# Optimization experiments

Measured on AMD Instinct MI355X. Metric: run time of the kernel, lower is better.

The kernel has to match this reference:

```python
import jax, jax.numpy as jnp
import numpy as np

N_EMBD = 256
BLOCK_SIZE = 128
N_HEAD = 8
HEAD_SIZE = 256
B = 256
T = 128


def setup_inputs() -> dict:
    key = jax.random.key(0)
    ks = jax.random.split(key, 9)
    s = 0.02
    return {
        "x": jax.random.normal(ks[0], (B, T, N_EMBD), dtype=jnp.float32),
        # torch Linear weight layout: [out_features, in_features], stacked over heads
        "Wq": jax.random.normal(ks[1], (N_HEAD, HEAD_SIZE, N_EMBD), dtype=jnp.float32) * s,
        "bq": jax.random.normal(ks[2], (N_HEAD, HEAD_SIZE), dtype=jnp.float32) * s,
        "Wk": jax.random.normal(ks[3], (N_HEAD, HEAD_SIZE, N_EMBD), dtype=jnp.float32) * s,
        "bk": jax.random.normal(ks[4], (N_HEAD, HEAD_SIZE), dtype=jnp.float32) * s,
        "Wv": jax.random.normal(ks[5], (N_HEAD, HEAD_SIZE, N_EMBD), dtype=jnp.float32) * s,
        "bv": jax.random.normal(ks[6], (N_HEAD, HEAD_SIZE), dtype=jnp.float32) * s,
        "Wp": jax.random.normal(ks[7], (N_EMBD, N_EMBD), dtype=jnp.float32) * s,
        "bp": jax.random.normal(ks[8], (N_EMBD,), dtype=jnp.float32) * s,
    }


def reference(x, Wq, bq, Wk, bk, Wv, bv, Wp, bp):
    Bb, Tt, C = x.shape
    scale = C ** (-0.5)  # NOTE: original scales by n_embd (input C), not head_size
    # per-head projections: [h, b, t, d]
    q = jnp.einsum("btc,hdc->hbtd", x, Wq) + bq[:, None, None, :]
    k = jnp.einsum("btc,hdc->hbtd", x, Wk) + bk[:, None, None, :]
    v = jnp.einsum("btc,hdc->hbtd", x, Wv) + bv[:, None, None, :]
    att = jnp.einsum("hbtd,hbsd->hbts", q, k) * scale  # [h,b,t,s]
    causal = jnp.tril(jnp.ones((Tt, Tt), dtype=bool))
    att = jnp.where(causal, att, -jnp.inf)
    att = jax.nn.softmax(att, axis=-1)
    out = jnp.einsum("hbts,hbsd->hbtd", att, v)
    # torch.cat along dim=0 (batch concat, as written in the source)
    out = out.reshape(out.shape[0] * Bb, Tt, out.shape[-1])  # [h*b, t, head_size]
    return out @ Wp.T + bp
```

## Files before the change

### kernel.cpp

```cpp
#include <hip/hip_runtime.h>
#include <hip/hip_bf16.h>
#include <stdint.h>


#define TT 128

typedef __attribute__((ext_vector_type(8))) short short8;
typedef __attribute__((ext_vector_type(4))) float f32x4;

#define WS_X    0u
#define WS_M    16777216u
#define WS_WM   17825792u
#define WS_WB   18874368u
#define WS_BB   18939904u
#define WS_CQ   18948096u

#define LX     0
#define LT     65536
#define LP     65536
#define LH     98304
#define R_UV   131072
#define R_RED  132096
#define LDS_SIZE 134144

#define VMCNT0() asm volatile("s_waitcnt vmcnt(0)" ::: "memory")
#define LGKM0()  asm volatile("s_waitcnt lgkmcnt(0)" ::: "memory")
#define BAR()    do { asm volatile("" ::: "memory"); __builtin_amdgcn_s_barrier(); asm volatile("" ::: "memory"); } while (0)
#define PRIO1()  __builtin_amdgcn_s_setprio(1)
#define PRIO0()  __builtin_amdgcn_s_setprio(0)

typedef __attribute__((address_space(3))) uint32_t lds_u32;
typedef __attribute__((address_space(1))) const uint32_t glb_u32;

__device__ __forceinline__ unsigned short f2bf(float x) {
    union { float f; unsigned u; } v; v.f = x;
    unsigned r = v.u + 0x7FFFu + ((v.u >> 16) & 1u);
    return (unsigned short)(r >> 16);
}
__device__ __forceinline__ unsigned pk2(float a, float b) {
    return (unsigned)f2bf(a) | ((unsigned)f2bf(b) << 16);
}

__global__ __launch_bounds__(256) void convert_pre(
    const float* __restrict__ x,
    const float* __restrict__ Wq, const float* __restrict__ bq,
    const float* __restrict__ Wk, const float* __restrict__ bk,
    const float* __restrict__ Wv, const float* __restrict__ bv,
    const float* __restrict__ Wp, const float* __restrict__ bp,
    char* __restrict__ ws)
{
    extern __shared__ char clds[];
    const int tid = threadIdx.x;
    const int bid = blockIdx.x;

    if (bid < 256) {
        const float* src = x + (size_t)bid * 32768;
        char* dst = ws + WS_X + (size_t)bid * 65536;
        for (int i = tid; i < 8192; i += 256) {
            float4 v = ((const float4*)src)[i];
            int row = i >> 6, c4 = i & 63;
            uint2 u; u.x = pk2(v.x, v.y); u.y = pk2(v.z, v.w);
            *(uint2*)(clds + row * 512 + ((c4 * 8) ^ ((row & 7) << 4))) = u;
        }
        __syncthreads();
        for (int i = tid; i < 4096; i += 256) {
            int l = i & 63, ks = (i >> 6) & 7, g = i >> 9;
            int r = g * 16 + (l & 15);
            int boff = ks * 64 + (l >> 4) * 16;
            uint4 q = *(const uint4*)(clds + r * 512 + (boff ^ ((r & 7) << 4)));
            ((uint4*)dst)[i] = q;
        }
        return;
    }
    if (bid < 384) {
        int id = bid - 256, h = id >> 4, st = id & 15;
        float* wkL = (float*)clds;
        for (int i = tid; i < 4096; i += 256) {
            int d = i >> 4, cc = i & 15;
            wkL[i] = Wk[(size_t)h * 65536 + d * 256 + st * 16 + cc];
        }
        __syncthreads();
        const int c = tid;
        float4 a0 = {0,0,0,0}, a1 = {0,0,0,0}, a2 = {0,0,0,0}, a3 = {0,0,0,0};
        const float4* wk4 = (const float4*)wkL;
        #pragma unroll 4
        for (int d = 0; d < 256; ++d) {
            float a = Wq[(size_t)h * 65536 + d * 256 + c];
            float4 k0 = wk4[d*4+0], k1 = wk4[d*4+1], k2 = wk4[d*4+2], k3 = wk4[d*4+3];
            a0.x += a*k0.x; a0.y += a*k0.y; a0.z += a*k0.z; a0.w += a*k0.w;
            a1.x += a*k1.x; a1.y += a*k1.y; a1.z += a*k1.z; a1.w += a*k1.w;
            a2.x += a*k2.x; a2.y += a*k2.y; a2.z += a*k2.z; a2.w += a*k2.w;
            a3.x += a*k3.x; a3.y += a*k3.y; a3.z += a*k3.z; a3.w += a*k3.w;
        }
        float acc[16] = {a0.x,a0.y,a0.z,a0.w, a1.x,a1.y,a1.z,a1.w,
                         a2.x,a2.y,a2.z,a2.w, a3.x,a3.y,a3.z,a3.w};
        char* base = ws + WS_M + (size_t)h * 131072;
        int ks = c >> 5, lgp = (c >> 3) & 3, jb = c & 7;
        #pragma unroll
        for (int j = 0; j < 16; ++j) {
            int cp = st * 16 + j;
            *(unsigned short*)(base + (((st * 8 + ks)) << 10)
                + ((cp & 15) + 16 * lgp) * 16 + jb * 2) = f2bf(acc[j] * 0.0625f);
        }
        return;
    }
    if (bid < 512) {
        int id = bid - 384, h = id >> 4, st = id & 15;
        float* wpT2 = (float*)clds;
        for (int i = tid; i < 1024; i += 256) {
            int e = i >> 6, d4 = i & 63;
            float4 v = ((const float4*)(Wp + (size_t)(st * 16 + e) * 256))[d4];
            int d = d4 * 4;
            wpT2[(d+0)*20+e] = v.x; wpT2[(d+1)*20+e] = v.y;
            wpT2[(d+2)*20+e] = v.z; wpT2[(d+3)*20+e] = v.w;
        }
        __syncthreads();
        const int c = tid;
        float4 a0 = {0,0,0,0}, a1 = {0,0,0,0}, a2 = {0,0,0,0}, a3 = {0,0,0,0};
        #pragma unroll 4
        for (int d = 0; d < 256; ++d) {
            float wv = Wv[(size_t)h * 65536 + d * 256 + c];
            const float4* wp4 = (const float4*)(wpT2 + d * 20);
            float4 p0 = wp4[0], p1 = wp4[1], p2 = wp4[2], p3 = wp4[3];
            a0.x += wv*p0.x; a0.y += wv*p0.y; a0.z += wv*p0.z; a0.w += wv*p0.w;
            a1.x += wv*p1.x; a1.y += wv*p1.y; a1.z += wv*p1.z; a1.w += wv*p1.w;
            a2.x += wv*p2.x; a2.y += wv*p2.y; a2.z += wv*p2.z; a2.w += wv*p2.w;
            a3.x += wv*p3.x; a3.y += wv*p3.y; a3.z += wv*p3.z; a3.w += wv*p3.w;
        }
        float acc[16] = {a0.x,a0.y,a0.z,a0.w, a1.x,a1.y,a1.z,a1.w,
                         a2.x,a2.y,a2.z,a2.w, a3.x,a3.y,a3.z,a3.w};
        char* base = ws + WS_WM + (size_t)h * 131072;
        int ks = c >> 5, lgp = (c >> 3) & 3, jb = c & 7;
        #pragma unroll
        for (int j = 0; j < 16; ++j) {
            *(unsigned short*)(base + (((st * 8 + ks)) << 10)
                + (j + 16 * lgp) * 16 + jb * 2) = f2bf(acc[j]);
        }
        return;
    }
    if (bid < 520) {
        const int h = bid - 512;
        {
            uint4 z = {0u,0u,0u,0u};
            for (int i = tid; i < 512; i += 256)
                ((uint4*)(ws + WS_WB + (size_t)h * 8192))[i] = z;
        }
        float* tK = (float*)clds;
        float* tQ = (float*)(clds + 16384);
        const int c = tid;
        float s1 = 0.f, s2 = 0.f;
        for (int d0 = 0; d0 < 256; d0 += 16) {
            __syncthreads();
            for (int i = tid; i < 1024; i += 256) {
                int row = i >> 6, c4 = i & 63;
                ((float4*)tK)[row * 64 + c4] =
                    ((const float4*)(Wk + (size_t)h * 65536 + (size_t)(d0 + row) * 256))[c4];
                ((float4*)tQ)[row * 64 + c4] =
                    ((const float4*)(Wq + (size_t)h * 65536 + (size_t)(d0 + row) * 256))[c4];
            }
            __syncthreads();
            #pragma unroll
            for (int dd = 0; dd < 16; ++dd) {
                s1 += tK[dd * 256 + c] * bq[h * 256 + d0 + dd];
                s2 += tQ[dd * 256 + c] * bk[h * 256 + d0 + dd];
            }
        }
        int ks = c >> 5, lgp = (c >> 3) & 3, jb = c & 7;
        char* base = ws + WS_WB + (size_t)h * 8192 + ks * 1024;
        *(unsigned short*)(base + (0 + 16 * lgp) * 16 + jb * 2) = f2bf(s2 * 0.0625f);
        *(unsigned short*)(base + (1 + 16 * lgp) * 16 + jb * 2) = f2bf(s1 * 0.0625f);
        float* red = (float*)(clds + 32768);
        red[tid] = bq[h * 256 + tid] * bk[h * 256 + tid];
        __syncthreads();
        if (tid == 0) {
            float cq = 0.f;
            for (int d = 0; d < 256; ++d) cq += red[d];
            *(float*)(ws + WS_CQ + h * 4) = cq * 0.0625f;
        }
        return;
    }
    {
        const int st = bid - 520;
        float* wpT = (float*)clds;
        float* bvL = (float*)(clds + 17408);
        for (int i = tid; i < 1024; i += 256) {
            int row = i >> 6, c4 = i & 63;
            float4 v = ((const float4*)(Wp + (size_t)(st * 16 + row) * 256))[c4];
            float* dstp = wpT + row * 257 + c4 * 4;
            dstp[0] = v.x; dstp[1] = v.y; dstp[2] = v.z; dstp[3] = v.w;
        }
        for (int i = tid; i < 512; i += 256)
            ((float4*)bvL)[i] = ((const float4*)bv)[i];
        __syncthreads();
        const int el = tid >> 4, dg = tid & 15;
        #pragma unroll
        for (int h = 0; h < 8; ++h) {
            float p = 0.f;
            #pragma unroll
            for (int dd = 0; dd < 16; ++dd) {
                int d = dg * 16 + dd;
                p += bvL[h * 256 + d] * wpT[el * 257 + d];
            }
            p += __shfl_xor(p, 1);
            p += __shfl_xor(p, 2);
            p += __shfl_xor(p, 4);
            p += __shfl_xor(p, 8);
            if (dg == 0)
                *(float*)(ws + WS_BB + (size_t)h * 1024 + (st * 16 + el) * 4)
                    = bp[st * 16 + el] + p;
        }
        return;
    }
}

__global__ __launch_bounds__(1024, 1) void mha_fused(
    const char* __restrict__ ws, float* __restrict__ out)
{
    extern __shared__ char lds[];
    const int tid = threadIdx.x;
    const int w  = tid >> 6, l = tid & 63;
    const int lg = l >> 4, lr = l & 15;
    const int mq = w & 7, nh = w >> 3;
    const int bid = blockIdx.x;
    const int xcd = bid & 7, j = bid >> 3;
    const int h = j & 7;
    const int b = ((j >> 3) << 3) | xcd;
    const size_t orow = ((size_t)(h * 256 + b)) * TT;

    const char* Xf  = ws + WS_X  + (size_t)b * 65536;
    const char* Mh  = ws + WS_M  + (size_t)h * 131072;
    const char* WMh = ws + WS_WM + (size_t)h * 131072;
    const char* WBh = ws + WS_WB + (size_t)h * 8192;

    {
        const char* src = Xf + tid * 16;
        #pragma unroll
        for (int p = 0; p < 4; ++p)
            __builtin_amdgcn_global_load_lds((glb_u32*)(src + p * 16384),
                (lds_u32*)(lds + LX + tid * 16 + p * 16384), 16, 0, 0);
    }
    VMCNT0(); BAR();

    if (nh == 0) {
        f32x4 vacc = f32x4{0.f,0.f,0.f,0.f};
        #pragma unroll
        for (int ks = 0; ks < 8; ++ks) {
            short8 wb = *(const short8*)(WBh + (ks << 10) + l*16);
            short8 xa = *(const short8*)(lds + LX + (((mq*8 + ks)) << 10) + l*16);
            vacc = __builtin_amdgcn_mfma_f32_16x16x32_bf16(xa, wb, vacc, 0, 0, 0);
        }
        if (lr < 2) {
            #pragma unroll
            for (int r = 0; r < 4; ++r) {
                int t = mq*16 + lg*4 + r;
                *(float*)(lds + R_UV + lr*512 + t*4) = vacc[r];
            }
        }
    }

    {
        const int th = w >> 3, cp = w & 7;
        f32x4 acc[4][2];
        #pragma unroll
        for (int i = 0; i < 4; ++i)
            #pragma unroll
            for (int c2 = 0; c2 < 2; ++c2) acc[i][c2] = f32x4{0.f,0.f,0.f,0.f};
        #pragma unroll
        for (int ks = 0; ks < 8; ++ks) {
            short8 nb[2];
            #pragma unroll
            for (int c2 = 0; c2 < 2; ++c2)
                nb[c2] = *(const short8*)(Mh + ((((cp*2+c2)*8 + ks)) << 10) + l*16);
            short8 xa[4];
            #pragma unroll
            for (int i = 0; i < 4; ++i)
                xa[i] = *(const short8*)(lds + LX + ((((th*4+i)*8 + ks)) << 10) + l*16);
            PRIO1();
            #pragma unroll
            for (int i = 0; i < 4; ++i)
                #pragma unroll
                for (int c2 = 0; c2 < 2; ++c2)
                    acc[i][c2] = __builtin_amdgcn_mfma_f32_16x16x32_bf16(xa[i], nb[c2], acc[i][c2], 0, 0, 0);
            PRIO0();
        }
        #pragma unroll
        for (int i = 0; i < 4; ++i)
            #pragma unroll
            for (int c2 = 0; c2 < 2; ++c2)
                #pragma unroll
                for (int r = 0; r < 4; ++r) {
                    int t = (th*4+i)*16 + lg*4 + r;
                    int c = (cp*2+c2)*16 + lr;
                    *(unsigned short*)(lds + LT + t*512 + ((c*2) ^ ((t&7)<<4)))
                        = f2bf(acc[i][c2][r]);
                }
    }
    LGKM0(); BAR();

    f32x4 sacc[4];
    #pragma unroll
    for (int i = 0; i < 4; ++i) sacc[i] = f32x4{0.f,0.f,0.f,0.f};
    #pragma unroll
    for (int ks2 = 0; ks2 < 8; ++ks2) {
        int t2 = mq*16 + lr;
        short8 ta = *(const short8*)(lds + LT + t2*512 + ((ks2*64 + lg*16) ^ ((t2&7)<<4)));
        short8 sb[4];
        #pragma unroll
        for (int nt = 0; nt < 4; ++nt)
            sb[nt] = *(const short8*)(lds + LX + (((nh*4+nt)*8 + ks2) << 10) + l*16);
        PRIO1();
        #pragma unroll
        for (int nt = 0; nt < 4; ++nt)
            sacc[nt] = __builtin_amdgcn_mfma_f32_16x16x32_bf16(ta, sb[nt], sacc[nt], 0, 0, 0);
        PRIO0();
    }

    {
        const float cq = *(const float*)(ws + WS_CQ + h*4);
        float uu[4];
        #pragma unroll
        for (int nt = 0; nt < 4; ++nt)
            uu[nt] = *(const float*)(lds + R_UV + 512 + (nh*64 + nt*16 + lr)*4);
        float* redM = (float*)(lds + R_RED);
        float* redS = redM + 256;
        float rmax[4];
        #pragma unroll
        for (int r = 0; r < 4; ++r) {
            int t = mq*16 + lg*4 + r;
            float vt = *(const float*)(lds + R_UV + t*4) + cq;
            float m = -1e30f;
            #pragma unroll
            for (int nt = 0; nt < 4; ++nt) {
                int s = nh*64 + nt*16 + lr;
                float sv = sacc[nt][r] + vt + uu[nt];
                if (s > t) sv = -1e30f;
                sacc[nt][r] = sv;
                m = fmaxf(m, sv);
            }
            m = fmaxf(m, __shfl_xor(m, 1));
            m = fmaxf(m, __shfl_xor(m, 2));
            m = fmaxf(m, __shfl_xor(m, 4));
            m = fmaxf(m, __shfl_xor(m, 8));
            rmax[r] = m;
        }
        if (lr == 0) {
            #pragma unroll
            for (int r = 0; r < 4; ++r)
                redM[nh*128 + mq*16 + lg*4 + r] = rmax[r];
        }
        LGKM0(); BAR();
        float rsum[4];
        #pragma unroll
        for (int r = 0; r < 4; ++r) {
            int t = mq*16 + lg*4 + r;
            float m = fmaxf(redM[t], redM[128 + t]);
            float ssum = 0.f;
            #pragma unroll
            for (int nt = 0; nt < 4; ++nt) {
                float p = __expf(sacc[nt][r] - m);
                sacc[nt][r] = p;
                ssum += p;
            }
            ssum += __shfl_xor(ssum, 1);
            ssum += __shfl_xor(ssum, 2);
            ssum += __shfl_xor(ssum, 4);
            ssum += __shfl_xor(ssum, 8);
            rsum[r] = ssum;
        }
        if (lr == 0) {
            #pragma unroll
            for (int r = 0; r < 4; ++r)
                redS[nh*128 + mq*16 + lg*4 + r] = rsum[r];
        }
        LGKM0(); BAR();
        #pragma unroll
        for (int r = 0; r < 4; ++r) {
            int t = mq*16 + lg*4 + r;
            float inv = 1.0f / (redS[t] + redS[128 + t]);
            #pragma unroll
            for (int nt = 0; nt < 4; ++nt) {
                int s = nh*64 + nt*16 + lr;
                *(unsigned short*)(lds + LP + t*256 + ((s*2) ^ ((t&7)<<4)))
                    = f2bf(sacc[nt][r] * inv);
            }
        }
    }
    LGKM0(); BAR();

    short8 pa[4];
    {
        int t2 = mq*16 + lr;
        #pragma unroll
        for (int ks = 0; ks < 4; ++ks)
            pa[ks] = *(const short8*)(lds + LP + t2*256 + ((ks*64 + lg*16) ^ ((t2&7)<<4)));
    }

    const float* bbp = (const float*)(ws + WS_BB + h*1024);
    #pragma unroll
    for (int eh = 0; eh < 2; ++eh) {
        {
            const int ep = w & 3, sp = w >> 2;
            f32x4 acc[2][2];
            #pragma unroll
            for (int i = 0; i < 2; ++i)
                #pragma unroll
                for (int c2 = 0; c2 < 2; ++c2) acc[i][c2] = f32x4{0.f,0.f,0.f,0.f};
            #pragma unroll
            for (int ks = 0; ks < 8; ++ks) {
                short8 wa[2];
                #pragma unroll
                for (int i = 0; i < 2; ++i)
                    wa[i] = *(const short8*)(WMh + ((((eh*8 + ep*2+i)*8 + ks)) << 10) + l*16);
                short8 sb[2];
                #pragma unroll
                for (int c2 = 0; c2 < 2; ++c2)
                    sb[c2] = *(const short8*)(lds + LX + ((((sp*2+c2)*8 + ks)) << 10) + l*16);
                PRIO1();
                #pragma unroll
                for (int i = 0; i < 2; ++i)
                    #pragma unroll
                    for (int c2 = 0; c2 < 2; ++c2)
                        acc[i][c2] = __builtin_amdgcn_mfma_f32_16x16x32_bf16(wa[i], sb[c2], acc[i][c2], 0, 0, 0);
                PRIO0();
            }
            #pragma unroll
            for (int i = 0; i < 2; ++i)
                #pragma unroll
                for (int c2 = 0; c2 < 2; ++c2)
                    #pragma unroll
                    for (int r = 0; r < 4; ++r) {
                        int el = (ep*2+i)*16 + lg*4 + r;
                        int s  = (sp*2+c2)*16 + lr;
                        *(unsigned short*)(lds + LH + el*256 + ((s*2) ^ ((el&7)<<4)))
                            = f2bf(acc[i][c2][r]);
                    }
        }
        LGKM0(); BAR();
        #pragma unroll
        for (int ec = 0; ec < 2; ++ec) {
            f32x4 acc[2];
            acc[0] = f32x4{0.f,0.f,0.f,0.f};
            acc[1] = f32x4{0.f,0.f,0.f,0.f};
            #pragma unroll
            for (int ks = 0; ks < 4; ++ks) {
                short8 hb[2];
                #pragma unroll
                for (int nt = 0; nt < 2; ++nt) {
                    int erl = nh*64 + (ec*2 + nt)*16 + lr;
                    hb[nt] = *(const short8*)(lds + LH + erl*256 + ((ks*64 + lg*16) ^ ((erl&7)<<4)));
                }
                PRIO1();
                #pragma unroll
                for (int nt = 0; nt < 2; ++nt)
                    acc[nt] = __builtin_amdgcn_mfma_f32_16x16x32_bf16(pa[ks], hb[nt], acc[nt], 0, 0, 0);
                PRIO0();
            }
            #pragma unroll
            for (int nt = 0; nt < 2; ++nt) {
                int e = eh*128 + nh*64 + (ec*2 + nt)*16 + lr;
                float bbv = bbp[e];
                #pragma unroll
                for (int r = 0; r < 4; ++r) {
                    int t = mq*16 + lg*4 + r;
                    out[(orow + t) * 256 + e] = acc[nt][r] + bbv;
                }
            }
        }
        if (eh == 0) { LGKM0(); BAR(); }
    }
}

extern "C" void kernel_launch(void* const* d_in, const int* in_sizes, int n_in,
                              void* d_out, int out_size, void* d_ws, size_t ws_size,
                              hipStream_t stream) {
    (void)in_sizes; (void)n_in; (void)out_size; (void)ws_size;
    const float* x  = (const float*)d_in[0];
    const float* Wq = (const float*)d_in[1];
    const float* bq = (const float*)d_in[2];
    const float* Wk = (const float*)d_in[3];
    const float* bk = (const float*)d_in[4];
    const float* Wv = (const float*)d_in[5];
    const float* bv = (const float*)d_in[6];
    const float* Wp = (const float*)d_in[7];
    const float* bp = (const float*)d_in[8];
    char* ws = (char*)d_ws;

    hipFuncSetAttribute((const void*)convert_pre,
                        hipFuncAttributeMaxDynamicSharedMemorySize, 65536);
    convert_pre<<<dim3(536), dim3(256), 65536, stream>>>(
        x, Wq, bq, Wk, bk, Wv, bv, Wp, bp, ws);

    hipFuncSetAttribute((const void*)mha_fused,
                        hipFuncAttributeMaxDynamicSharedMemorySize, LDS_SIZE);
    mha_fused<<<dim3(2048), dim3(1024), LDS_SIZE, stream>>>(ws, (float*)d_out);
}
```

Measured before the change: 236.3 us.

## Overlap first V-projection phase with softmax reductions and stage weights via LDS

In the fused attention kernel, the first half of the H = X·WM projection (ph2(0)) now runs between the softmax max and sum reductions, sharing a barrier instead of running after the softmax. This hides barrier and reduction latency behind MFMA work and removes one barrier. In the preprocessing kernel, Wq and Wv rows are loaded in coalesced 16-row tiles into LDS instead of per-thread strided global loads. f2bf now uses the native __bf16 conversion. The LH region must not alias the regions the softmax still reads, or results will be corrupted.

Measured after the change: 233.8 us (median of 2 runs). No clear change (-1.0%).

```diff
diff --git a/kernel.cpp b/kernel.cpp
--- a/kernel.cpp
+++ b/kernel.cpp
@@ -33,9 +33,9 @@
 typedef __attribute__((address_space(1))) const uint32_t glb_u32;
 
 __device__ __forceinline__ unsigned short f2bf(float x) {
-    union { float f; unsigned u; } v; v.f = x;
-    unsigned r = v.u + 0x7FFFu + ((v.u >> 16) & 1u);
-    return (unsigned short)(r >> 16);
+    union { __bf16 b; unsigned short u; } v;
+    v.b = (__bf16)x;
+    return v.u;
 }
 __device__ __forceinline__ unsigned pk2(float a, float b) {
     return (unsigned)f2bf(a) | ((unsigned)f2bf(b) << 16);
@@ -75,22 +75,32 @@
     if (bid < 384) {
         int id = bid - 256, h = id >> 4, st = id & 15;
         float* wkL = (float*)clds;
+        float* wqT = (float*)(clds + 16384);
         for (int i = tid; i < 4096; i += 256) {
             int d = i >> 4, cc = i & 15;
             wkL[i] = Wk[(size_t)h * 65536 + d * 256 + st * 16 + cc];
         }
-        __syncthreads();
         const int c = tid;
         float4 a0 = {0,0,0,0}, a1 = {0,0,0,0}, a2 = {0,0,0,0}, a3 = {0,0,0,0};
         const float4* wk4 = (const float4*)wkL;
-        #pragma unroll 4
-        for (int d = 0; d < 256; ++d) {
-            float a = Wq[(size_t)h * 65536 + d * 256 + c];
-            float4 k0 = wk4[d*4+0], k1 = wk4[d*4+1], k2 = wk4[d*4+2], k3 = wk4[d*4+3];
-            a0.x += a*k0.x; a0.y += a*k0.y; a0.z += a*k0.z; a0.w += a*k0.w;
-            a1.x += a*k1.x; a1.y += a*k1.y; a1.z += a*k1.z; a1.w += a*k1.w;
-            a2.x += a*k2.x; a2.y += a*k2.y; a2.z += a*k2.z; a2.w += a*k2.w;
-            a3.x += a*k3.x; a3.y += a*k3.y; a3.z += a*k3.z; a3.w += a*k3.w;
+        for (int d0 = 0; d0 < 256; d0 += 16) {
+            __syncthreads();
+            for (int i = tid; i < 1024; i += 256) {
+                int row = i >> 6, c4 = i & 63;
+                ((float4*)wqT)[row * 64 + c4] =
+                    ((const float4*)(Wq + (size_t)h * 65536 + (size_t)(d0 + row) * 256))[c4];
+            }
+            __syncthreads();
+            #pragma unroll
+            for (int dd = 0; dd < 16; ++dd) {
+                int d = d0 + dd;
+                float a = wqT[dd * 256 + c];
+                float4 k0 = wk4[d*4+0], k1 = wk4[d*4+1], k2 = wk4[d*4+2], k3 = wk4[d*4+3];
+                a0.x += a*k0.x; a0.y += a*k0.y; a0.z += a*k0.z; a0.w += a*k0.w;
+                a1.x += a*k1.x; a1.y += a*k1.y; a1.z += a*k1.z; a1.w += a*k1.w;
+                a2.x += a*k2.x; a2.y += a*k2.y; a2.z += a*k2.z; a2.w += a*k2.w;
+                a3.x += a*k3.x; a3.y += a*k3.y; a3.z += a*k3.z; a3.w += a*k3.w;
+            }
         }
         float acc[16] = {a0.x,a0.y,a0.z,a0.w, a1.x,a1.y,a1.z,a1.w,
                          a2.x,a2.y,a2.z,a2.w, a3.x,a3.y,a3.z,a3.w};
@@ -107,6 +117,7 @@
     if (bid < 512) {
         int id = bid - 384, h = id >> 4, st = id & 15;
         float* wpT2 = (float*)clds;
+        float* wvT  = (float*)(clds + 20480);
         for (int i = tid; i < 1024; i += 256) {
             int e = i >> 6, d4 = i & 63;
             float4 v = ((const float4*)(Wp + (size_t)(st * 16 + e) * 256))[d4];
@@ -114,18 +125,27 @@
             wpT2[(d+0)*20+e] = v.x; wpT2[(d+1)*20+e] = v.y;
             wpT2[(d+2)*20+e] = v.z; wpT2[(d+3)*20+e] = v.w;
         }
-        __syncthreads();
         const int c = tid;
         float4 a0 = {0,0,0,0}, a1 = {0,0,0,0}, a2 = {0,0,0,0}, a3 = {0,0,0,0};
-        #pragma unroll 4
-        for (int d = 0; d < 256; ++d) {
-            float wv = Wv[(size_t)h * 65536 + d * 256 + c];
-            const float4* wp4 = (const float4*)(wpT2 + d * 20);
-            float4 p0 = wp4[0], p1 = wp4[1], p2 = wp4[2], p3 = wp4[3];
-            a0.x += wv*p0.x; a0.y += wv*p0.y; a0.z += wv*p0.z; a0.w += wv*p0.w;
-            a1.x += wv*p1.x; a1.y += wv*p1.y; a1.z += wv*p1.z; a1.w += wv*p1.w;
-            a2.x += wv*p2.x; a2.y += wv*p2.y; a2.z += wv*p2.z; a2.w += wv*p2.w;
-            a3.x += wv*p3.x; a3.y += wv*p3.y; a3.z += wv*p3.z; a3.w += wv*p3.w;
+        for (int d0 = 0; d0 < 256; d0 += 16) {
+            __syncthreads();
+            for (int i = tid; i < 1024; i += 256) {
+                int row = i >> 6, c4 = i & 63;
+                ((float4*)wvT)[row * 64 + c4] =
+                    ((const float4*)(Wv + (size_t)h * 65536 + (size_t)(d0 + row) * 256))[c4];
+            }
+            __syncthreads();
+            #pragma unroll
+            for (int dd = 0; dd < 16; ++dd) {
+                int d = d0 + dd;
+                float wv = wvT[dd * 256 + c];
+                const float4* wp4 = (const float4*)(wpT2 + d * 20);
+                float4 p0 = wp4[0], p1 = wp4[1], p2 = wp4[2], p3 = wp4[3];
+                a0.x += wv*p0.x; a0.y += wv*p0.y; a0.z += wv*p0.z; a0.w += wv*p0.w;
+                a1.x += wv*p1.x; a1.y += wv*p1.y; a1.z += wv*p1.z; a1.w += wv*p1.w;
+                a2.x += wv*p2.x; a2.y += wv*p2.y; a2.z += wv*p2.z; a2.w += wv*p2.w;
+                a3.x += wv*p3.x; a3.y += wv*p3.y; a3.z += wv*p3.z; a3.w += wv*p3.w;
+            }
         }
         float acc[16] = {a0.x,a0.y,a0.z,a0.w, a1.x,a1.y,a1.z,a1.w,
                          a2.x,a2.y,a2.z,a2.w, a3.x,a3.y,a3.z,a3.w};
@@ -221,6 +241,7 @@
     const int w  = tid >> 6, l = tid & 63;
     const int lg = l >> 4, lr = l & 15;
     const int mq = w & 7, nh = w >> 3;
+    const int ep = w & 3, sp = w >> 2;
     const int bid = blockIdx.x;
     const int xcd = bid & 7, j = bid >> 3;
     const int h = j & 7;
@@ -231,6 +252,76 @@
     const char* Mh  = ws + WS_M  + (size_t)h * 131072;
     const char* WMh = ws + WS_WM + (size_t)h * 131072;
     const char* WBh = ws + WS_WB + (size_t)h * 8192;
+
+    auto ph2 = [&](int eh) {
+        f32x4 acc[2][2];
+        #pragma unroll
+        for (int i = 0; i < 2; ++i)
+            #pragma unroll
+            for (int c2 = 0; c2 < 2; ++c2) acc[i][c2] = f32x4{0.f,0.f,0.f,0.f};
+        #pragma unroll
+        for (int ks = 0; ks < 8; ++ks) {
+            short8 wa[2];
+            #pragma unroll
+            for (int i = 0; i < 2; ++i)
+                wa[i] = *(const short8*)(WMh + ((((eh*8 + ep*2+i)*8 + ks)) << 10) + l*16);
+            short8 sb[2];
+            #pragma unroll
+            for (int c2 = 0; c2 < 2; ++c2)
+                sb[c2] = *(const short8*)(lds + LX + ((((sp*2+c2)*8 + ks)) << 10) + l*16);
+            PRIO1();
+            #pragma unroll
+            for (int i = 0; i < 2; ++i)
+                #pragma unroll
+                for (int c2 = 0; c2 < 2; ++c2)
+                    acc[i][c2] = __builtin_amdgcn_mfma_f32_16x16x32_bf16(wa[i], sb[c2], acc[i][c2], 0, 0, 0);
+            PRIO0();
+        }
+        #pragma unroll
+        for (int i = 0; i < 2; ++i)
+            #pragma unroll
+            for (int c2 = 0; c2 < 2; ++c2)
+                #pragma unroll
+                for (int r = 0; r < 4; ++r) {
+                    int el = (ep*2+i)*16 + lg*4 + r;
+                    int s  = (sp*2+c2)*16 + lr;
+                    *(unsigned short*)(lds + LH + el*256 + ((s*2) ^ ((el&7)<<4)))
+                        = f2bf(acc[i][c2][r]);
+                }
+    };
+    const float* bbp = (const float*)(ws + WS_BB + h*1024);
+    auto ph3 = [&](int eh, const short8* pa) {
+        #pragma unroll
+        for (int ec = 0; ec < 2; ++ec) {
+            f32x4 acc[2];
+            acc[0] = f32x4{0.f,0.f,0.f,0.f};
+            acc[1] = f32x4{0.f,0.f,0.f,0.f};
+            #pragma unroll
+            for (int ks = 0; ks < 4; ++ks) {
+                short8 hb[2];
+                #pragma unroll
+                for (int nt = 0; nt < 2; ++nt) {
+                    int erl = nh*64 + (ec*2 + nt)*16 + lr;
+                    hb[nt] = *(const short8*)(lds + LH + erl*256 + ((ks*64 + lg*16) ^ ((erl&7)<<4)));
+                }
+                PRIO1();
+                #pragma unroll
+                for (int nt = 0; nt < 2; ++nt)
+                    acc[nt] = __builtin_amdgcn_mfma_f32_16x16x32_bf16(pa[ks], hb[nt], acc[nt], 0, 0, 0);
+                PRIO0();
+            }
+            #pragma unroll
+            for (int nt = 0; nt < 2; ++nt) {
+                int e = eh*128 + nh*64 + (ec*2 + nt)*16 + lr;
+                float bbv = bbp[e];
+                #pragma unroll
+                for (int r = 0; r < 4; ++r) {
+                    int t = mq*16 + lg*4 + r;
+                    out[(orow + t) * 256 + e] = acc[nt][r] + bbv;
+                }
+            }
+        }
+    };
 
     {
         const char* src = Xf + tid * 16;
@@ -314,15 +405,14 @@
             sacc[nt] = __builtin_amdgcn_mfma_f32_16x16x32_bf16(ta, sb[nt], sacc[nt], 0, 0, 0);
         PRIO0();
     }
-
+    float* redM = (float*)(lds + R_RED);
+    float* redS = redM + 256;
     {
         const float cq = *(const float*)(ws + WS_CQ + h*4);
         float uu[4];
         #pragma unroll
         for (int nt = 0; nt < 4; ++nt)
             uu[nt] = *(const float*)(lds + R_UV + 512 + (nh*64 + nt*16 + lr)*4);
-        float* redM = (float*)(lds + R_RED);
-        float* redS = redM + 256;
         float rmax[4];
         #pragma unroll
         for (int r = 0; r < 4; ++r) {
@@ -348,7 +438,11 @@
             for (int r = 0; r < 4; ++r)
                 redM[nh*128 + mq*16 + lg*4 + r] = rmax[r];
         }
-        LGKM0(); BAR();
+    }
+    LGKM0(); BAR();
+
+    ph2(0);
+    {
         float rsum[4];
         #pragma unroll
         for (int r = 0; r < 4; ++r) {
@@ -372,17 +466,18 @@
             for (int r = 0; r < 4; ++r)
                 redS[nh*128 + mq*16 + lg*4 + r] = rsum[r];
         }
-        LGKM0(); BAR();
-        #pragma unroll
-        for (int r = 0; r < 4; ++r) {
-            int t = mq*16 + lg*4 + r;
-            float inv = 1.0f / (redS[t] + redS[128 + t]);
-            #pragma unroll
-            for (int nt = 0; nt < 4; ++nt) {
-                int s = nh*64 + nt*16 + lr;
-                *(unsigned short*)(lds + LP + t*256 + ((s*2) ^ ((t&7)<<4)))
-                    = f2bf(sacc[nt][r] * inv);
-            }
+    }
+    LGKM0(); BAR();
+
+    #pragma unroll
+    for (int r = 0; r < 4; ++r) {
+        int t = mq*16 + lg*4 + r;
+        float inv = 1.0f / (redS[t] + redS[128 + t]);
+        #pragma unroll
+        for (int nt = 0; nt < 4; ++nt) {
+            int s = nh*64 + nt*16 + lr;
+            *(unsigned short*)(lds + LP + t*256 + ((s*2) ^ ((t&7)<<4)))
+                = f2bf(sacc[nt][r] * inv);
         }
     }
     LGKM0(); BAR();
@@ -394,80 +489,12 @@
         for (int ks = 0; ks < 4; ++ks)
             pa[ks] = *(const short8*)(lds + LP + t2*256 + ((ks*64 + lg*16) ^ ((t2&7)<<4)));
     }
-
-    const float* bbp = (const float*)(ws + WS_BB + h*1024);
-    #pragma unroll
-    for (int eh = 0; eh < 2; ++eh) {
-        {
-            const int ep = w & 3, sp = w >> 2;
-            f32x4 acc[2][2];
-            #pragma unroll
-            for (int i = 0; i < 2; ++i)
-                #pragma unroll
-                for (int c2 = 0; c2 < 2; ++c2) acc[i][c2] = f32x4{0.f,0.f,0.f,0.f};
-            #pragma unroll
-            for (int ks = 0; ks < 8; ++ks) {
-                short8 wa[2];
-                #pragma unroll
-                for (int i = 0; i < 2; ++i)
-                    wa[i] = *(const short8*)(WMh + ((((eh*8 + ep*2+i)*8 + ks)) << 10) + l*16);
-                short8 sb[2];
-                #pragma unroll
-                for (int c2 = 0; c2 < 2; ++c2)
-                    sb[c2] = *(const short8*)(lds + LX + ((((sp*2+c2)*8 + ks)) << 10) + l*16);
-                PRIO1();
-                #pragma unroll
-                for (int i = 0; i < 2; ++i)
-                    #pragma unroll
-                    for (int c2 = 0; c2 < 2; ++c2)
-                        acc[i][c2] = __builtin_amdgcn_mfma_f32_16x16x32_bf16(wa[i], sb[c2], acc[i][c2], 0, 0, 0);
-                PRIO0();
-            }
-            #pragma unroll
-            for (int i = 0; i < 2; ++i)
-                #pragma unroll
-                for (int c2 = 0; c2 < 2; ++c2)
-                    #pragma unroll
-                    for (int r = 0; r < 4; ++r) {
-                        int el = (ep*2+i)*16 + lg*4 + r;
-                        int s  = (sp*2+c2)*16 + lr;
-                        *(unsigned short*)(lds + LH + el*256 + ((s*2) ^ ((el&7)<<4)))
-                            = f2bf(acc[i][c2][r]);
-                    }
-        }
-        LGKM0(); BAR();
-        #pragma unroll
-        for (int ec = 0; ec < 2; ++ec) {
-            f32x4 acc[2];
-            acc[0] = f32x4{0.f,0.f,0.f,0.f};
-            acc[1] = f32x4{0.f,0.f,0.f,0.f};
-            #pragma unroll
-            for (int ks = 0; ks < 4; ++ks) {
-                short8 hb[2];
-                #pragma unroll
-                for (int nt = 0; nt < 2; ++nt) {
-                    int erl = nh*64 + (ec*2 + nt)*16 + lr;
-                    hb[nt] = *(const short8*)(lds + LH + erl*256 + ((ks*64 + lg*16) ^ ((erl&7)<<4)));
-                }
-                PRIO1();
-                #pragma unroll
-                for (int nt = 0; nt < 2; ++nt)
-                    acc[nt] = __builtin_amdgcn_mfma_f32_16x16x32_bf16(pa[ks], hb[nt], acc[nt], 0, 0, 0);
-                PRIO0();
-            }
-            #pragma unroll
-            for (int nt = 0; nt < 2; ++nt) {
-                int e = eh*128 + nh*64 + (ec*2 + nt)*16 + lr;
-                float bbv = bbp[e];
-                #pragma unroll
-                for (int r = 0; r < 4; ++r) {
-                    int t = mq*16 + lg*4 + r;
-                    out[(orow + t) * 256 + e] = acc[nt][r] + bbv;
-                }
-            }
-        }
-        if (eh == 0) { LGKM0(); BAR(); }
-    }
+    ph3(0, pa);
+    LGKM0(); BAR();
+
+    ph2(1);
+    LGKM0(); BAR();
+    ph3(1, pa);
 }
 
 extern "C" void kernel_launch(void* const* d_in, const int* in_sizes, int n_in,
```
